# Kernel tuning notes

Hardware: AMD Instinct MI355X
Metric: run time of the kernel (lower is better)

The kernel has to match this reference:

```python
import jax, jax.numpy as jnp
import numpy as np

B, S, D, H = 4, 2048, 768, 12
HD = D // H
SCALE = HD ** -0.5


def setup_inputs() -> dict:
    key = jax.random.key(0)
    ks = jax.random.split(key, 9)
    std = D ** -0.5
    x = jax.random.normal(ks[0], (B, S, D), dtype=jnp.float32)
    Wq = jax.random.normal(ks[1], (D, D), dtype=jnp.float32) * std
    Wk = jax.random.normal(ks[2], (D, D), dtype=jnp.float32) * std
    Wv = jax.random.normal(ks[3], (D, D), dtype=jnp.float32) * std
    Wo = jax.random.normal(ks[4], (D, D), dtype=jnp.float32) * std
    bq = jax.random.normal(ks[5], (D,), dtype=jnp.float32) * 0.01
    bk = jax.random.normal(ks[6], (D,), dtype=jnp.float32) * 0.01
    bv = jax.random.normal(ks[7], (D,), dtype=jnp.float32) * 0.01
    bo = jax.random.normal(ks[8], (D,), dtype=jnp.float32) * 0.01
    return {"x": x, "Wq": Wq, "bq": bq, "Wk": Wk, "bk": bk,
            "Wv": Wv, "bv": bv, "Wo": Wo, "bo": bo}


def reference(x, Wq, bq, Wk, bk, Wv, bv, Wo, bo):
    b, s, _ = x.shape
    # projections (torch Linear: y = x @ W.T + b)
    q = (x @ Wq.T + bq).reshape(b, s, H, HD).transpose(0, 2, 1, 3)  # [B,H,S,HD]
    k = (x @ Wk.T + bk).reshape(b, s, H, HD).transpose(0, 2, 1, 3)
    v = (x @ Wv.T + bv).reshape(b, s, H, HD).transpose(0, 2, 1, 3)
    attn = jnp.einsum('bhqd,bhkd->bhqk', q, k) * SCALE
    attn = jax.nn.softmax(attn, axis=-1)  # dropout is identity in eval mode
    out = jnp.einsum('bhqk,bhkd->bhqd', attn, v)
    out = out.transpose(0, 2, 1, 3).reshape(b, s, D)
    return out @ Wo.T + bo
```

## Files before the change

### kernel.cpp

```cpp
#include <hip/hip_runtime.h>

#define LOG2E 1.4426950408889634f
#define QSCALE (0.125f * LOG2E)

typedef __attribute__((ext_vector_type(8))) __bf16 bf8_t;
typedef __attribute__((ext_vector_type(4))) float f4_t;

__device__ __forceinline__ unsigned short f2bf(float f) {
  unsigned int u = __float_as_uint(f);
  u += 0x7fff + ((u >> 16) & 1);
  return (unsigned short)(u >> 16);
}

__device__ __forceinline__ void async16(const void* g, void* l) {
  __builtin_amdgcn_global_load_lds(
      (const __attribute__((address_space(1))) void*)g,
      (__attribute__((address_space(3))) void*)l, 16, 0, 0);
}

__device__ __forceinline__ int swm(int r) {
  return ((r & 3) << 4) | ((r & 8) << 3);
}
__device__ __forceinline__ int swzoff(int row, int cb) {
  return (row << 7) + (cb ^ swm(row));
}

__global__ void cvt_multi(const float* __restrict__ x,
                          const float* __restrict__ w0, const float* __restrict__ w1,
                          const float* __restrict__ w2, const float* __restrict__ w3,
                          unsigned short* __restrict__ xb,
                          unsigned short* __restrict__ d0, unsigned short* __restrict__ d1,
                          unsigned short* __restrict__ d2, unsigned short* __restrict__ d3) {
  const int NX = 1572864;
  const int NW = 147456;
  const int total = NX + 4 * NW;
  int i = blockIdx.x * blockDim.x + threadIdx.x;
  int stride = gridDim.x * blockDim.x;
  for (; i < total; i += stride) {
    const float* s;
    unsigned short* d;
    int off;
    if (i < NX) {
      s = x; d = xb; off = i;
    } else {
      int j = i - NX;
      int wsel = j / NW;
      off = j - wsel * NW;
      s = (wsel == 0) ? w0 : (wsel == 1) ? w1 : (wsel == 2) ? w2 : w3;
      d = (wsel == 0) ? d0 : (wsel == 1) ? d1 : (wsel == 2) ? d2 : d3;
    }
    float4 v = ((const float4*)s)[off];
    ushort4 o;
    o.x = f2bf(v.x); o.y = f2bf(v.y); o.z = f2bf(v.z); o.w = f2bf(v.w);
    ((ushort4*)d)[off] = o;
  }
}

__device__ __forceinline__ void gemm_core(const unsigned short* __restrict__ A,
                                          const unsigned short* __restrict__ Bm,
                                          int i0, int j0, char* ls,
                                          f4_t (&acc)[4][4]) {
  const int tid = threadIdx.x;
  const int l = tid & 63;
  const int wi = (tid >> 6) >> 1, wj = (tid >> 6) & 1;
  auto stage = [&](int buf, int k0) {
    char* dA = ls + buf * 32768;
    char* dB = dA + 16384;
#pragma unroll
    for (int u = 0; u < 4; ++u) {
      int p = (u * 256 + tid) * 16;
      int r = p >> 7, c = (p & 127) ^ swm(r);
      async16((const char*)A + ((size_t)(i0 + r) * 768 + k0) * 2 + c, dA + p);
      async16((const char*)Bm + ((size_t)(j0 + r) * 768 + k0) * 2 + c, dB + p);
    }
  };
  stage(0, 0);
  for (int kk = 0; kk < 12; ++kk) {
    if (kk < 11) {
      stage((kk + 1) & 1, (kk + 1) * 64);
      asm volatile("s_waitcnt vmcnt(8)" ::: "memory");
    } else {
      asm volatile("s_waitcnt vmcnt(0)" ::: "memory");
    }
    __builtin_amdgcn_s_barrier();
    const char* lsA = ls + (kk & 1) * 32768;
    const char* lsB = lsA + 16384;
#pragma unroll
    for (int ks = 0; ks < 2; ++ks) {
      bf8_t af[4], bfr[4];
#pragma unroll
      for (int mi = 0; mi < 4; ++mi)
        af[mi] = *(const bf8_t*)(lsA + swzoff(wi * 64 + mi * 16 + (l & 15),
                                              ks * 64 + ((l >> 4) << 4)));
#pragma unroll
      for (int nj = 0; nj < 4; ++nj)
        bfr[nj] = *(const bf8_t*)(lsB + swzoff(wj * 64 + nj * 16 + (l & 15),
                                               ks * 64 + ((l >> 4) << 4)));
      __builtin_amdgcn_s_setprio(1);
#pragma unroll
      for (int mi = 0; mi < 4; ++mi)
#pragma unroll
        for (int nj = 0; nj < 4; ++nj)
          acc[mi][nj] = __builtin_amdgcn_mfma_f32_16x16x32_bf16(
              af[mi], bfr[nj], acc[mi][nj], 0, 0, 0);
      __builtin_amdgcn_s_setprio(0);
    }
    __builtin_amdgcn_s_barrier();
  }
}

__global__ __launch_bounds__(256) void proj_qkv(
    const unsigned short* __restrict__ xb,
    const unsigned short* __restrict__ wq,
    const unsigned short* __restrict__ wk,
    const unsigned short* __restrict__ wv,
    const float* __restrict__ bq, const float* __restrict__ bk,
    const float* __restrict__ bv,
    unsigned short* __restrict__ qo, unsigned short* __restrict__ ko,
    unsigned short* __restrict__ vto) {
  __shared__ char ls[65536];
  const int bx = (blockIdx.x & 7) * 144 + (blockIdx.x >> 3);
  const int mt = bx / 18, nt = bx % 18;
  const int sec = nt / 6, nn = nt % 6;
  const int nbase = nn * 128;
  const int mbase = mt * 128;
  const unsigned short *A, *Bm;
  if (sec == 0)      { A = wq; Bm = xb; }
  else if (sec == 1) { A = wk; Bm = xb; }
  else               { A = xb; Bm = wv; }
  const int gi0 = (sec == 2) ? mbase : nbase;
  const int gj0 = (sec == 2) ? nbase : mbase;
  f4_t acc[4][4] = {};
  gemm_core(A, Bm, gi0, gj0, ls, acc);

  const int tid = threadIdx.x, l = tid & 63;
  const int wi = (tid >> 6) >> 1, wj = (tid >> 6) & 1;
#pragma unroll
  for (int mi = 0; mi < 4; ++mi) {
#pragma unroll
    for (int nj = 0; nj < 4; ++nj) {
      int ib = wi * 64 + mi * 16 + ((l >> 4) << 2);
      int j  = wj * 64 + nj * 16 + (l & 15);
      f4_t v = acc[mi][nj];
      ushort4 o;
      if (sec < 2) {
        const float* bias = sec ? bk : bq;
        float sc = sec ? 1.0f : QSCALE;
        float4 bs = *(const float4*)(bias + nbase + ib);
        o.x = f2bf((v[0] + bs.x) * sc);
        o.y = f2bf((v[1] + bs.y) * sc);
        o.z = f2bf((v[2] + bs.z) * sc);
        o.w = f2bf((v[3] + bs.w) * sc);
      } else {
        float bvs = bv[nbase + j];
        o.x = f2bf(v[0] + bvs); o.y = f2bf(v[1] + bvs);
        o.z = f2bf(v[2] + bvs); o.w = f2bf(v[3] + bvs);
      }
      int chunk = (ib >> 3) ^ (j & 15);
      *(ushort4*)(ls + j * 256 + chunk * 16 + ((ib & 7) << 1)) = o;
    }
  }
  __syncthreads();
  const int row = tid >> 1, half = tid & 1;
  if (sec < 2) {
    int sg = mbase + row;
    int b = sg >> 11, s = sg & 2047;
    int h = nn * 2 + half;
    unsigned short* dst = (sec ? ko : qo) + (((size_t)(b * 12 + h) * 2048 + s) << 6);
#pragma unroll
    for (int c = 0; c < 8; ++c) {
      int cb = half * 8 + c;
      uint4 v = *(const uint4*)(ls + row * 256 + ((cb ^ (row & 15)) << 4));
      ((uint4*)dst)[c] = v;
    }
  } else {
    int h = nn * 2 + (row >> 6), dh = row & 63;
    int b = mt >> 4;
    int scol = (mt & 15) * 128 + half * 64;
    unsigned short* dst = vto + ((size_t)((b * 12 + h) * 64 + dh)) * 2048 + scol;
#pragma unroll
    for (int c = 0; c < 8; ++c) {
      int cb = half * 8 + c;
      uint4 v = *(const uint4*)(ls + row * 256 + ((cb ^ (row & 15)) << 4));
      ((uint4*)dst)[c] = v;
    }
  }
}

__global__ __launch_bounds__(256) void proj_o(
    const unsigned short* __restrict__ attnb, const unsigned short* __restrict__ wo,
    const float* __restrict__ bo, float* __restrict__ outp) {
  __shared__ char ls[65536];
  const int bx = (blockIdx.x & 7) * 48 + (blockIdx.x >> 3);
  const int it = bx % 6, jt = bx / 6;
  const int i0 = it * 128, j0 = jt * 128;
  f4_t acc[4][4] = {};
  gemm_core(wo, attnb, i0, j0, ls, acc);
  const int tid = threadIdx.x, l = tid & 63;
  const int wi = (tid >> 6) >> 1, wj = (tid >> 6) & 1;
#pragma unroll
  for (int mi = 0; mi < 4; ++mi) {
#pragma unroll
    for (int nj = 0; nj < 4; ++nj) {
      int ib = i0 + wi * 64 + mi * 16 + ((l >> 4) << 2);
      int j  = j0 + wj * 64 + nj * 16 + (l & 15);
      float4 bs = *(const float4*)(bo + ib);
      float4 o;
      o.x = acc[mi][nj][0] + bs.x;
      o.y = acc[mi][nj][1] + bs.y;
      o.z = acc[mi][nj][2] + bs.z;
      o.w = acc[mi][nj][3] + bs.w;
      *(float4*)(outp + (size_t)j * 768 + ib) = o;
    }
  }
}

__global__ __launch_bounds__(512) void attn_kernel(
    const unsigned short* __restrict__ qg,
    const unsigned short* __restrict__ kg,
    const unsigned short* __restrict__ vtg,
    unsigned short* __restrict__ attnb) {
  __shared__ char ls[65536];
  const int tid = threadIdx.x, l = tid & 63, w = tid >> 6;
  const int qw = w & 3, hf = w >> 2;
  const int swz = (blockIdx.x & 7) * 96 + (blockIdx.x >> 3);
  const int q0 = (swz & 15) * 128;
  const int bh = swz >> 4;
  const size_t qkbase = (size_t)bh * 2048 * 64;
  const size_t vtbase = (size_t)bh * 64 * 2048;

#pragma unroll
  for (int u = 0; u < 2; ++u) {
    int p = (u * 512 + tid) * 16;
    int r = p >> 7, cb = p & 127;
    int c = cb ^ swm(r);
    async16((const char*)qg + (qkbase + (size_t)(q0 + r) * 64) * 2 + c, ls + p);
  }
  __syncthreads();
  bf8_t qf[2][2];
#pragma unroll
  for (int qt = 0; qt < 2; ++qt)
#pragma unroll
    for (int ks = 0; ks < 2; ++ks)
      qf[qt][ks] = *(const bf8_t*)(ls + swzoff(qw * 32 + qt * 16 + (l & 15),
                                               ks * 64 + ((l >> 4) << 4)));
  __syncthreads();

  const int p16 = tid * 16;
  const int sr = p16 >> 7;
  const int sc = (p16 & 127) ^ swm(sr);
  async16((const char*)kg + (qkbase + (size_t)sr * 64) * 2 + sc, ls + p16);
  async16((const char*)vtg + (vtbase + (size_t)sr * 2048) * 2 + sc,
          ls + 8192 + p16);
  async16((const char*)kg + (qkbase + (size_t)(64 + sr) * 64) * 2 + sc,
          ls + 16384 + p16);
  async16((const char*)vtg + (vtbase + (size_t)sr * 2048 + 64) * 2 + sc,
          ls + 16384 + 8192 + p16);
  const char* gKa = (const char*)kg + (qkbase + (size_t)(128 + sr) * 64) * 2 + sc;
  const char* gVa = (const char*)vtg + (vtbase + (size_t)sr * 2048 + 128) * 2 + sc;
  const char* gKb = gKa + 8192;
  const char* gVb = gVa + 128;

  int koff[4][2];
#pragma unroll
  for (int kt = 0; kt < 4; ++kt) {
    int i = l & 15;
    int row = ((kt >> 1) << 5) + ((kt & 1) << 2) + ((i >> 2) << 3) + (i & 3);
#pragma unroll
    for (int ks = 0; ks < 2; ++ks)
      koff[kt][ks] = swzoff(row, ks * 64 + ((l >> 4) << 4));
  }
  int voff[4][2];
#pragma unroll
  for (int dt = 0; dt < 4; ++dt)
#pragma unroll
    for (int ks = 0; ks < 2; ++ks)
      voff[dt][ks] = swzoff(dt * 16 + (l & 15), ks * 64 + ((l >> 4) << 4));

  bf8_t onesf;
#pragma unroll
  for (int e = 0; e < 8; ++e) onesf[e] = (__bf16)1.0f;

  f4_t acc[4][2] = {};
  f4_t accs[2] = {};

  for (int i = 0; i < 16; ++i) {
    if (i < 15) {
      char* dst = ls + (((i + 1) & 1) * 2) * 16384;
      async16(gKa, dst + p16);
      async16(gVa, dst + 8192 + p16);
      async16(gKb, dst + 16384 + p16);
      async16(gVb, dst + 16384 + 8192 + p16);
      gKa += 16384; gKb += 16384;
      gVa += 256;   gVb += 256;
      asm volatile("s_waitcnt vmcnt(4)" ::: "memory");
    } else {
      asm volatile("s_waitcnt vmcnt(0)" ::: "memory");
    }
    __builtin_amdgcn_s_barrier();
    const char* bK = ls + ((i & 1) * 2 + hf) * 16384;
    const char* bV = bK + 8192;

    f4_t sacc[4][2] = {};
    __builtin_amdgcn_s_setprio(1);
#pragma unroll
    for (int kt = 0; kt < 4; ++kt)
#pragma unroll
      for (int ks = 0; ks < 2; ++ks) {
        bf8_t a = *(const bf8_t*)(bK + koff[kt][ks]);
#pragma unroll
        for (int qt = 0; qt < 2; ++qt)
          sacc[kt][qt] = __builtin_amdgcn_mfma_f32_16x16x32_bf16(
              a, qf[qt][ks], sacc[kt][qt], 0, 0, 0);
      }
    __builtin_amdgcn_s_setprio(0);

    bf8_t pf[2][2];
#pragma unroll
    for (int qt = 0; qt < 2; ++qt)
#pragma unroll
      for (int ks = 0; ks < 2; ++ks)
#pragma unroll
        for (int e = 0; e < 8; ++e)
          pf[ks][qt][e] =
              (__bf16)__builtin_amdgcn_exp2f(sacc[2 * ks + (e >> 2)][qt][e & 3]);

    __builtin_amdgcn_s_setprio(1);
#pragma unroll
    for (int dt = 0; dt < 4; ++dt) {
      bf8_t av0 = *(const bf8_t*)(bV + voff[dt][0]);
      bf8_t av1 = *(const bf8_t*)(bV + voff[dt][1]);
#pragma unroll
      for (int qt = 0; qt < 2; ++qt) {
        acc[dt][qt] = __builtin_amdgcn_mfma_f32_16x16x32_bf16(av0, pf[0][qt],
                                                              acc[dt][qt], 0, 0, 0);
        acc[dt][qt] = __builtin_amdgcn_mfma_f32_16x16x32_bf16(av1, pf[1][qt],
                                                              acc[dt][qt], 0, 0, 0);
      }
    }
#pragma unroll
    for (int qt = 0; qt < 2; ++qt) {
      accs[qt] = __builtin_amdgcn_mfma_f32_16x16x32_bf16(onesf, pf[0][qt],
                                                         accs[qt], 0, 0, 0);
      accs[qt] = __builtin_amdgcn_mfma_f32_16x16x32_bf16(onesf, pf[1][qt],
                                                         accs[qt], 0, 0, 0);
    }
    __builtin_amdgcn_s_setprio(0);
    __builtin_amdgcn_s_barrier();
  }

  char* reg_ = ls + qw * 8704;
  if (hf) {
#pragma unroll
    for (int dt = 0; dt < 4; ++dt)
#pragma unroll
      for (int qt = 0; qt < 2; ++qt)
        *(f4_t*)(reg_ + (((dt * 2 + qt) * 64) + l) * 16) = acc[dt][qt];
    *(float2*)(reg_ + 8192 + l * 8) = float2{accs[0][0], accs[1][0]};
  }
  __syncthreads();
  if (!hf) {
    const int bb = bh / 12, h = bh % 12;
    float2 os = *(const float2*)(reg_ + 8192 + l * 8);
    float inv0 = 1.0f / (accs[0][0] + os.x);
    float inv1 = 1.0f / (accs[1][0] + os.y);
#pragma unroll
    for (int qt = 0; qt < 2; ++qt) {
      float inv = qt ? inv1 : inv0;
      int s = q0 + qw * 32 + qt * 16 + (l & 15);
#pragma unroll
      for (int dt = 0; dt < 4; ++dt) {
        f4_t other = *(const f4_t*)(reg_ + (((dt * 2 + qt) * 64) + l) * 16);
        int dg = h * 64 + dt * 16 + ((l >> 4) << 2);
        ushort4 o;
        o.x = f2bf((acc[dt][qt][0] + other[0]) * inv);
        o.y = f2bf((acc[dt][qt][1] + other[1]) * inv);
        o.z = f2bf((acc[dt][qt][2] + other[2]) * inv);
        o.w = f2bf((acc[dt][qt][3] + other[3]) * inv);
        *(ushort4*)(attnb + ((size_t)(bb * 2048 + s)) * 768 + dg) = o;
      }
    }
  }
}

extern "C" void kernel_launch(void* const* d_in, const int* in_sizes, int n_in,
                              void* d_out, int out_size, void* d_ws, size_t ws_size,
                              hipStream_t stream) {
  const float* x  = (const float*)d_in[0];
  const float* Wq = (const float*)d_in[1];
  const float* bq = (const float*)d_in[2];
  const float* Wk = (const float*)d_in[3];
  const float* bk = (const float*)d_in[4];
  const float* Wv = (const float*)d_in[5];
  const float* bv = (const float*)d_in[6];
  const float* Wo = (const float*)d_in[7];
  const float* bo = (const float*)d_in[8];

  const size_t XB_ELEMS = (size_t)8192 * 768;
  const size_t W_ELEMS  = (size_t)768 * 768;
  unsigned short* xb  = (unsigned short*)d_ws;
  unsigned short* wqb = xb  + XB_ELEMS;
  unsigned short* wkb = wqb + W_ELEMS;
  unsigned short* wvb = wkb + W_ELEMS;
  unsigned short* wob = wvb + W_ELEMS;
  unsigned short* qb  = wob + W_ELEMS;
  unsigned short* kb  = qb  + XB_ELEMS;
  unsigned short* vtb = kb  + XB_ELEMS;
  unsigned short* attnb = xb;

  cvt_multi<<<2048, 256, 0, stream>>>(x, Wq, Wk, Wv, Wo,
                                      xb, wqb, wkb, wvb, wob);
  proj_qkv<<<1152, 256, 0, stream>>>(xb, wqb, wkb, wvb, bq, bk, bv, qb, kb, vtb);
  attn_kernel<<<768, 512, 0, stream>>>(qb, kb, vtb, attnb);
  proj_o<<<384, 256, 0, stream>>>(attnb, wob, bo, (float*)d_out);
}
```

Before: 137.2 us.

## Software-pipeline softmax and PV across iterations for second-half waves

Waves with hf set now compute QK scores for the current tile and buffer them with V fragments in registers, then run exp2 and PV for the previous tile in the next iteration. The other half keeps the original order, so the two wave groups sit in different phases and their MFMA and transcendental work can interleave. In exchange the hf waves hold extra registers for the previous scores and V fragments, which can hurt occupancy, and the loop gains a drain step after it ends.

```diff
diff --git a/kernel.cpp b/kernel.cpp
--- a/kernel.cpp
+++ b/kernel.cpp
@@ -283,6 +283,39 @@
 
   f4_t acc[4][2] = {};
   f4_t accs[2] = {};
+  f4_t psacc[4][2];
+  bf8_t pvf[4][2];
+
+  auto do_sm = [&](f4_t (&sc)[4][2], bf8_t (&pf)[2][2]) {
+#pragma unroll
+    for (int qt = 0; qt < 2; ++qt)
+#pragma unroll
+      for (int ks = 0; ks < 2; ++ks)
+#pragma unroll
+        for (int e = 0; e < 8; ++e)
+          pf[ks][qt][e] =
+              (__bf16)__builtin_amdgcn_exp2f(sc[2 * ks + (e >> 2)][qt][e & 3]);
+  };
+  auto do_pv = [&](bf8_t (&pf)[2][2], bf8_t (&av)[4][2]) {
+    __builtin_amdgcn_s_setprio(1);
+#pragma unroll
+    for (int dt = 0; dt < 4; ++dt)
+#pragma unroll
+      for (int qt = 0; qt < 2; ++qt) {
+        acc[dt][qt] = __builtin_amdgcn_mfma_f32_16x16x32_bf16(av[dt][0], pf[0][qt],
+                                                              acc[dt][qt], 0, 0, 0);
+        acc[dt][qt] = __builtin_amdgcn_mfma_f32_16x16x32_bf16(av[dt][1], pf[1][qt],
+                                                              acc[dt][qt], 0, 0, 0);
+      }
+#pragma unroll
+    for (int qt = 0; qt < 2; ++qt) {
+      accs[qt] = __builtin_amdgcn_mfma_f32_16x16x32_bf16(onesf, pf[0][qt],
+                                                         accs[qt], 0, 0, 0);
+      accs[qt] = __builtin_amdgcn_mfma_f32_16x16x32_bf16(onesf, pf[1][qt],
+                                                         accs[qt], 0, 0, 0);
+    }
+    __builtin_amdgcn_s_setprio(0);
+  };
 
   for (int i = 0; i < 16; ++i) {
     if (i < 15) {
@@ -301,52 +334,64 @@
     const char* bK = ls + ((i & 1) * 2 + hf) * 16384;
     const char* bV = bK + 8192;
 
-    f4_t sacc[4][2] = {};
-    __builtin_amdgcn_s_setprio(1);
-#pragma unroll
-    for (int kt = 0; kt < 4; ++kt)
-#pragma unroll
-      for (int ks = 0; ks < 2; ++ks) {
-        bf8_t a = *(const bf8_t*)(bK + koff[kt][ks]);
+    if (!hf) {
+      f4_t sacc[4][2] = {};
+      __builtin_amdgcn_s_setprio(1);
+#pragma unroll
+      for (int kt = 0; kt < 4; ++kt)
+#pragma unroll
+        for (int ks = 0; ks < 2; ++ks) {
+          bf8_t a = *(const bf8_t*)(bK + koff[kt][ks]);
+#pragma unroll
+          for (int qt = 0; qt < 2; ++qt)
+            sacc[kt][qt] = __builtin_amdgcn_mfma_f32_16x16x32_bf16(
+                a, qf[qt][ks], sacc[kt][qt], 0, 0, 0);
+        }
+      __builtin_amdgcn_s_setprio(0);
+      bf8_t pf[2][2];
+      do_sm(sacc, pf);
+      bf8_t av[4][2];
+#pragma unroll
+      for (int dt = 0; dt < 4; ++dt) {
+        av[dt][0] = *(const bf8_t*)(bV + voff[dt][0]);
+        av[dt][1] = *(const bf8_t*)(bV + voff[dt][1]);
+      }
+      do_pv(pf, av);
+    } else {
+      if (i > 0) {
+        bf8_t pf[2][2];
+        do_sm(psacc, pf);
+        do_pv(pf, pvf);
+      }
+#pragma unroll
+      for (int kt = 0; kt < 4; ++kt)
 #pragma unroll
         for (int qt = 0; qt < 2; ++qt)
-          sacc[kt][qt] = __builtin_amdgcn_mfma_f32_16x16x32_bf16(
-              a, qf[qt][ks], sacc[kt][qt], 0, 0, 0);
-      }
-    __builtin_amdgcn_s_setprio(0);
-
+          psacc[kt][qt] = f4_t{0.0f, 0.0f, 0.0f, 0.0f};
+      __builtin_amdgcn_s_setprio(1);
+#pragma unroll
+      for (int kt = 0; kt < 4; ++kt)
+#pragma unroll
+        for (int ks = 0; ks < 2; ++ks) {
+          bf8_t a = *(const bf8_t*)(bK + koff[kt][ks]);
+#pragma unroll
+          for (int qt = 0; qt < 2; ++qt)
+            psacc[kt][qt] = __builtin_amdgcn_mfma_f32_16x16x32_bf16(
+                a, qf[qt][ks], psacc[kt][qt], 0, 0, 0);
+        }
+      __builtin_amdgcn_s_setprio(0);
+#pragma unroll
+      for (int dt = 0; dt < 4; ++dt) {
+        pvf[dt][0] = *(const bf8_t*)(bV + voff[dt][0]);
+        pvf[dt][1] = *(const bf8_t*)(bV + voff[dt][1]);
+      }
+    }
+    __builtin_amdgcn_s_barrier();
+  }
+  if (hf) {
     bf8_t pf[2][2];
-#pragma unroll
-    for (int qt = 0; qt < 2; ++qt)
-#pragma unroll
-      for (int ks = 0; ks < 2; ++ks)
-#pragma unroll
-        for (int e = 0; e < 8; ++e)
-          pf[ks][qt][e] =
-              (__bf16)__builtin_amdgcn_exp2f(sacc[2 * ks + (e >> 2)][qt][e & 3]);
-
-    __builtin_amdgcn_s_setprio(1);
-#pragma unroll
-    for (int dt = 0; dt < 4; ++dt) {
-      bf8_t av0 = *(const bf8_t*)(bV + voff[dt][0]);
-      bf8_t av1 = *(const bf8_t*)(bV + voff[dt][1]);
-#pragma unroll
-      for (int qt = 0; qt < 2; ++qt) {
-        acc[dt][qt] = __builtin_amdgcn_mfma_f32_16x16x32_bf16(av0, pf[0][qt],
-                                                              acc[dt][qt], 0, 0, 0);
-        acc[dt][qt] = __builtin_amdgcn_mfma_f32_16x16x32_bf16(av1, pf[1][qt],
-                                                              acc[dt][qt], 0, 0, 0);
-      }
-    }
-#pragma unroll
-    for (int qt = 0; qt < 2; ++qt) {
-      accs[qt] = __builtin_amdgcn_mfma_f32_16x16x32_bf16(onesf, pf[0][qt],
-                                                         accs[qt], 0, 0, 0);
-      accs[qt] = __builtin_amdgcn_mfma_f32_16x16x32_bf16(onesf, pf[1][qt],
-                                                         accs[qt], 0, 0, 0);
-    }
-    __builtin_amdgcn_s_setprio(0);
-    __builtin_amdgcn_s_barrier();
+    do_sm(psacc, pf);
+    do_pv(pf, pvf);
   }
 
   char* reg_ = ls + qw * 8704;
```

Measured after the change: 149.1 us. +8.7%, slower.

## Retile output projection to 128x64 with double-buffered pipeline; simplify attention sync

Applied to the files above, without the earlier changes.

The output projection now uses 128x64 tiles, doubling the grid to 768 blocks for better load balance across CUs. It replaces the shared gemm_core with an inline double-buffered async-to-LDS K-loop that uses less LDS. The attention loop drops its explicit vmcnt wait and top-of-loop barrier, relying on a __syncthreads after the prologue and at the end of each iteration. Smaller tiles give less operand reuse per block. The sync change depends on __syncthreads draining outstanding LDS-direct loads, which may also stall on the prefetch earlier than before.

```diff
diff --git a/kernel.cpp b/kernel.cpp
--- a/kernel.cpp
+++ b/kernel.cpp
@@ -190,20 +190,68 @@
 __global__ __launch_bounds__(256) void proj_o(
     const unsigned short* __restrict__ attnb, const unsigned short* __restrict__ wo,
     const float* __restrict__ bo, float* __restrict__ outp) {
-  __shared__ char ls[65536];
-  const int bx = (blockIdx.x & 7) * 48 + (blockIdx.x >> 3);
+  __shared__ char ls[49152];
+  const int bx = (blockIdx.x & 7) * 96 + (blockIdx.x >> 3);
   const int it = bx % 6, jt = bx / 6;
-  const int i0 = it * 128, j0 = jt * 128;
-  f4_t acc[4][4] = {};
-  gemm_core(wo, attnb, i0, j0, ls, acc);
+  const int i0 = it * 128, j0 = jt * 64;
   const int tid = threadIdx.x, l = tid & 63;
   const int wi = (tid >> 6) >> 1, wj = (tid >> 6) & 1;
+  auto stage = [&](int buf, int k0) {
+    char* dA = ls + buf * 24576;
+    char* dB = dA + 16384;
+#pragma unroll
+    for (int u = 0; u < 4; ++u) {
+      int p = (u * 256 + tid) * 16;
+      int r = p >> 7, c = (p & 127) ^ swm(r);
+      async16((const char*)wo + ((size_t)(i0 + r) * 768 + k0) * 2 + c, dA + p);
+    }
+#pragma unroll
+    for (int u = 0; u < 2; ++u) {
+      int p = (u * 256 + tid) * 16;
+      int r = p >> 7, c = (p & 127) ^ swm(r);
+      async16((const char*)attnb + ((size_t)(j0 + r) * 768 + k0) * 2 + c, dB + p);
+    }
+  };
+  f4_t acc[4][2] = {};
+  stage(0, 0);
+  for (int kk = 0; kk < 12; ++kk) {
+    if (kk < 11) {
+      stage((kk + 1) & 1, (kk + 1) * 64);
+      asm volatile("s_waitcnt vmcnt(6)" ::: "memory");
+    } else {
+      asm volatile("s_waitcnt vmcnt(0)" ::: "memory");
+    }
+    __builtin_amdgcn_s_barrier();
+    const char* lsA = ls + (kk & 1) * 24576;
+    const char* lsB = lsA + 16384;
+#pragma unroll
+    for (int ks = 0; ks < 2; ++ks) {
+      bf8_t af[4], bfr[2];
+#pragma unroll
+      for (int mi = 0; mi < 4; ++mi)
+        af[mi] = *(const bf8_t*)(lsA + swzoff(wi * 64 + mi * 16 + (l & 15),
+                                              ks * 64 + ((l >> 4) << 4)));
+#pragma unroll
+      for (int nj = 0; nj < 2; ++nj)
+        bfr[nj] = *(const bf8_t*)(lsB + swzoff(wj * 32 + nj * 16 + (l & 15),
+                                               ks * 64 + ((l >> 4) << 4)));
+      __builtin_amdgcn_s_setprio(1);
+#pragma unroll
+      for (int mi = 0; mi < 4; ++mi)
+#pragma unroll
+        for (int nj = 0; nj < 2; ++nj)
+          acc[mi][nj] = __builtin_amdgcn_mfma_f32_16x16x32_bf16(
+              af[mi], bfr[nj], acc[mi][nj], 0, 0, 0);
+      __builtin_amdgcn_s_setprio(0);
+    }
+    __builtin_amdgcn_s_barrier();
+  }
 #pragma unroll
   for (int mi = 0; mi < 4; ++mi) {
 #pragma unroll
-    for (int nj = 0; nj < 4; ++nj) {
+    for (int nj = 0; nj < 2; ++nj) {
       int ib = i0 + wi * 64 + mi * 16 + ((l >> 4) << 2);
-      int j  = j0 + wj * 64 + nj * 16 + (l & 15);
+      int j  = j0 + wj * 32 + nj * 16 + (l & 15);
       float4 bs = *(const float4*)(bo + ib);
       float4 o;
       o.x = acc[mi][nj][0] + bs.x;
@@ -260,6 +308,7 @@
   const char* gVa = (const char*)vtg + (vtbase + (size_t)sr * 2048 + 128) * 2 + sc;
   const char* gKb = gKa + 8192;
   const char* gVb = gVa + 128;
+  __syncthreads();
 
   int koff[4][2];
 #pragma unroll
@@ -293,11 +342,7 @@
       async16(gVb, dst + 16384 + 8192 + p16);
       gKa += 16384; gKb += 16384;
       gVa += 256;   gVb += 256;
-      asm volatile("s_waitcnt vmcnt(4)" ::: "memory");
-    } else {
-      asm volatile("s_waitcnt vmcnt(0)" ::: "memory");
-    }
-    __builtin_amdgcn_s_barrier();
+    }
     const char* bK = ls + ((i & 1) * 2 + hf) * 16384;
     const char* bV = bK + 8192;
 
@@ -346,7 +391,7 @@
                                                          accs[qt], 0, 0, 0);
     }
     __builtin_amdgcn_s_setprio(0);
-    __builtin_amdgcn_s_barrier();
+    __syncthreads();
   }
 
   char* reg_ = ls + qw * 8704;
@@ -412,5 +457,5 @@
                                       xb, wqb, wkb, wvb, wob);
   proj_qkv<<<1152, 256, 0, stream>>>(xb, wqb, wkb, wvb, bq, bk, bv, qb, kb, vtb);
   attn_kernel<<<768, 512, 0, stream>>>(qb, kb, vtb, attnb);
-  proj_o<<<384, 256, 0, stream>>>(attnb, wob, bo, (float*)d_out);
-}
+  proj_o<<<768, 256, 0, stream>>>(attnb, wob, bo, (float*)d_out);
+}
```

After: 133.8 us. 1.02x faster.

## Shrink projection GEMM tiles to 128x64 and simplify attention loop synchronisation

Applied to the files above, without the earlier changes.

The QKV and output projection GEMMs move from 128x128 to 128x64 output tiles. That doubles the grid sizes, cuts shared memory per block from 64KB to 48KB and remaps the Q/K/V^T epilogue stores for the narrower tile. The aim is better occupancy and load balance across CUs, at the cost of less operand reuse per block. Separately, the attention loop drops its explicit vmcnt wait and barrier before compute and relies on a full __syncthreads at the end of each iteration, plus one before the loop. This makes correctness depend on __syncthreads draining outstanding async LDS loads.

```diff
diff --git a/kernel.cpp b/kernel.cpp
--- a/kernel.cpp
+++ b/kernel.cpp
@@ -56,21 +56,25 @@
   }
 }
 
-__device__ __forceinline__ void gemm_core(const unsigned short* __restrict__ A,
-                                          const unsigned short* __restrict__ Bm,
-                                          int i0, int j0, char* ls,
-                                          f4_t (&acc)[4][4]) {
-  const int tid = threadIdx.x;
-  const int l = tid & 63;
+__device__ __forceinline__ void gemm_core64(const unsigned short* __restrict__ A,
+                                            const unsigned short* __restrict__ Bm,
+                                            int i0, int j0, char* ls,
+                                            f4_t (&acc)[4][2]) {
+  const int tid = threadIdx.x, l = tid & 63;
   const int wi = (tid >> 6) >> 1, wj = (tid >> 6) & 1;
   auto stage = [&](int buf, int k0) {
-    char* dA = ls + buf * 32768;
+    char* dA = ls + buf * 24576;
     char* dB = dA + 16384;
 #pragma unroll
     for (int u = 0; u < 4; ++u) {
       int p = (u * 256 + tid) * 16;
       int r = p >> 7, c = (p & 127) ^ swm(r);
       async16((const char*)A + ((size_t)(i0 + r) * 768 + k0) * 2 + c, dA + p);
+    }
+#pragma unroll
+    for (int u = 0; u < 2; ++u) {
+      int p = (u * 256 + tid) * 16;
+      int r = p >> 7, c = (p & 127) ^ swm(r);
       async16((const char*)Bm + ((size_t)(j0 + r) * 768 + k0) * 2 + c, dB + p);
     }
   };
@@ -78,29 +82,29 @@
   for (int kk = 0; kk < 12; ++kk) {
     if (kk < 11) {
       stage((kk + 1) & 1, (kk + 1) * 64);
-      asm volatile("s_waitcnt vmcnt(8)" ::: "memory");
+      asm volatile("s_waitcnt vmcnt(6)" ::: "memory");
     } else {
       asm volatile("s_waitcnt vmcnt(0)" ::: "memory");
     }
     __builtin_amdgcn_s_barrier();
-    const char* lsA = ls + (kk & 1) * 32768;
+    const char* lsA = ls + (kk & 1) * 24576;
     const char* lsB = lsA + 16384;
 #pragma unroll
     for (int ks = 0; ks < 2; ++ks) {
-      bf8_t af[4], bfr[4];
+      bf8_t af[4], bfr[2];
 #pragma unroll
       for (int mi = 0; mi < 4; ++mi)
         af[mi] = *(const bf8_t*)(lsA + swzoff(wi * 64 + mi * 16 + (l & 15),
                                               ks * 64 + ((l >> 4) << 4)));
 #pragma unroll
-      for (int nj = 0; nj < 4; ++nj)
-        bfr[nj] = *(const bf8_t*)(lsB + swzoff(wj * 64 + nj * 16 + (l & 15),
+      for (int nj = 0; nj < 2; ++nj)
+        bfr[nj] = *(const bf8_t*)(lsB + swzoff(wj * 32 + nj * 16 + (l & 15),
                                                ks * 64 + ((l >> 4) << 4)));
       __builtin_amdgcn_s_setprio(1);
 #pragma unroll
       for (int mi = 0; mi < 4; ++mi)
 #pragma unroll
-        for (int nj = 0; nj < 4; ++nj)
+        for (int nj = 0; nj < 2; ++nj)
           acc[mi][nj] = __builtin_amdgcn_mfma_f32_16x16x32_bf16(
               af[mi], bfr[nj], acc[mi][nj], 0, 0, 0);
       __builtin_amdgcn_s_setprio(0);
@@ -118,41 +122,42 @@
     const float* __restrict__ bv,
     unsigned short* __restrict__ qo, unsigned short* __restrict__ ko,
     unsigned short* __restrict__ vto) {
-  __shared__ char ls[65536];
-  const int bx = (blockIdx.x & 7) * 144 + (blockIdx.x >> 3);
+  __shared__ char ls[49152];
+  const int bx = (blockIdx.x & 7) * 288 + (blockIdx.x >> 3);
   const int mt = bx / 18, nt = bx % 18;
   const int sec = nt / 6, nn = nt % 6;
-  const int nbase = nn * 128;
-  const int mbase = mt * 128;
-  const unsigned short *A, *Bm;
-  if (sec == 0)      { A = wq; Bm = xb; }
-  else if (sec == 1) { A = wk; Bm = xb; }
-  else               { A = xb; Bm = wv; }
-  const int gi0 = (sec == 2) ? mbase : nbase;
-  const int gj0 = (sec == 2) ? nbase : mbase;
-  f4_t acc[4][4] = {};
-  gemm_core(A, Bm, gi0, gj0, ls, acc);
+  f4_t acc[4][2] = {};
+  int i0, j0;
+  if (sec < 2) {
+    i0 = nn * 128;
+    j0 = mt * 64;
+    gemm_core64(sec ? wk : wq, xb, i0, j0, ls, acc);
+  } else {
+    i0 = (mt >> 1) * 128;
+    j0 = (nn * 2 + (mt & 1)) * 64;
+    gemm_core64(xb, wv, i0, j0, ls, acc);
+  }
 
   const int tid = threadIdx.x, l = tid & 63;
   const int wi = (tid >> 6) >> 1, wj = (tid >> 6) & 1;
 #pragma unroll
   for (int mi = 0; mi < 4; ++mi) {
 #pragma unroll
-    for (int nj = 0; nj < 4; ++nj) {
+    for (int nj = 0; nj < 2; ++nj) {
       int ib = wi * 64 + mi * 16 + ((l >> 4) << 2);
-      int j  = wj * 64 + nj * 16 + (l & 15);
+      int j  = wj * 32 + nj * 16 + (l & 15);
       f4_t v = acc[mi][nj];
       ushort4 o;
       if (sec < 2) {
         const float* bias = sec ? bk : bq;
         float sc = sec ? 1.0f : QSCALE;
-        float4 bs = *(const float4*)(bias + nbase + ib);
+        float4 bs = *(const float4*)(bias + i0 + ib);
         o.x = f2bf((v[0] + bs.x) * sc);
         o.y = f2bf((v[1] + bs.y) * sc);
         o.z = f2bf((v[2] + bs.z) * sc);
         o.w = f2bf((v[3] + bs.w) * sc);
       } else {
-        float bvs = bv[nbase + j];
+        float bvs = bv[j0 + j];
         o.x = f2bf(v[0] + bvs); o.y = f2bf(v[1] + bvs);
         o.z = f2bf(v[2] + bvs); o.w = f2bf(v[3] + bvs);
       }
@@ -161,28 +166,29 @@
     }
   }
   __syncthreads();
-  const int row = tid >> 1, half = tid & 1;
+  const int row = tid >> 2, q4 = tid & 3;
   if (sec < 2) {
-    int sg = mbase + row;
+    int sg = mt * 64 + row;
     int b = sg >> 11, s = sg & 2047;
-    int h = nn * 2 + half;
-    unsigned short* dst = (sec ? ko : qo) + (((size_t)(b * 12 + h) * 2048 + s) << 6);
-#pragma unroll
-    for (int c = 0; c < 8; ++c) {
-      int cb = half * 8 + c;
+    unsigned short* base = sec ? ko : qo;
+#pragma unroll
+    for (int cc = 0; cc < 4; ++cc) {
+      int cb = q4 * 4 + cc;
       uint4 v = *(const uint4*)(ls + row * 256 + ((cb ^ (row & 15)) << 4));
-      ((uint4*)dst)[c] = v;
+      int h = nn * 2 + (cb >> 3);
+      *(uint4*)(base + (((size_t)(b * 12 + h) * 2048 + s) << 6) + (cb & 7) * 8) = v;
     }
   } else {
-    int h = nn * 2 + (row >> 6), dh = row & 63;
-    int b = mt >> 4;
-    int scol = (mt & 15) * 128 + half * 64;
-    unsigned short* dst = vto + ((size_t)((b * 12 + h) * 64 + dh)) * 2048 + scol;
-#pragma unroll
-    for (int c = 0; c < 8; ++c) {
-      int cb = half * 8 + c;
+    int h = nn * 2 + (mt & 1), dh = row;
+    int st = mt >> 1;
+    int b = st >> 4;
+    int sl = (st & 15) * 128;
+    unsigned short* dst0 = vto + ((size_t)((b * 12 + h) * 64 + dh)) * 2048 + sl;
+#pragma unroll
+    for (int cc = 0; cc < 4; ++cc) {
+      int cb = q4 * 4 + cc;
       uint4 v = *(const uint4*)(ls + row * 256 + ((cb ^ (row & 15)) << 4));
-      ((uint4*)dst)[c] = v;
+      *(uint4*)(dst0 + cb * 8) = v;
     }
   }
 }
@@ -190,20 +196,20 @@
 __global__ __launch_bounds__(256) void proj_o(
     const unsigned short* __restrict__ attnb, const unsigned short* __restrict__ wo,
     const float* __restrict__ bo, float* __restrict__ outp) {
-  __shared__ char ls[65536];
-  const int bx = (blockIdx.x & 7) * 48 + (blockIdx.x >> 3);
+  __shared__ char ls[49152];
+  const int bx = (blockIdx.x & 7) * 96 + (blockIdx.x >> 3);
   const int it = bx % 6, jt = bx / 6;
-  const int i0 = it * 128, j0 = jt * 128;
-  f4_t acc[4][4] = {};
-  gemm_core(wo, attnb, i0, j0, ls, acc);
+  const int i0 = it * 128, j0 = jt * 64;
+  f4_t acc[4][2] = {};
+  gemm_core64(wo, attnb, i0, j0, ls, acc);
   const int tid = threadIdx.x, l = tid & 63;
   const int wi = (tid >> 6) >> 1, wj = (tid >> 6) & 1;
 #pragma unroll
   for (int mi = 0; mi < 4; ++mi) {
 #pragma unroll
-    for (int nj = 0; nj < 4; ++nj) {
+    for (int nj = 0; nj < 2; ++nj) {
       int ib = i0 + wi * 64 + mi * 16 + ((l >> 4) << 2);
-      int j  = j0 + wj * 64 + nj * 16 + (l & 15);
+      int j  = j0 + wj * 32 + nj * 16 + (l & 15);
       float4 bs = *(const float4*)(bo + ib);
       float4 o;
       o.x = acc[mi][nj][0] + bs.x;
@@ -260,6 +266,7 @@
   const char* gVa = (const char*)vtg + (vtbase + (size_t)sr * 2048 + 128) * 2 + sc;
   const char* gKb = gKa + 8192;
   const char* gVb = gVa + 128;
+  __syncthreads();
 
   int koff[4][2];
 #pragma unroll
@@ -293,11 +300,7 @@
       async16(gVb, dst + 16384 + 8192 + p16);
       gKa += 16384; gKb += 16384;
       gVa += 256;   gVb += 256;
-      asm volatile("s_waitcnt vmcnt(4)" ::: "memory");
-    } else {
-      asm volatile("s_waitcnt vmcnt(0)" ::: "memory");
-    }
-    __builtin_amdgcn_s_barrier();
+    }
     const char* bK = ls + ((i & 1) * 2 + hf) * 16384;
     const char* bV = bK + 8192;
 
@@ -346,7 +349,7 @@
                                                          accs[qt], 0, 0, 0);
     }
     __builtin_amdgcn_s_setprio(0);
-    __builtin_amdgcn_s_barrier();
+    __syncthreads();
   }
 
   char* reg_ = ls + qw * 8704;
@@ -410,7 +413,7 @@
 
   cvt_multi<<<2048, 256, 0, stream>>>(x, Wq, Wk, Wv, Wo,
                                       xb, wqb, wkb, wvb, wob);
-  proj_qkv<<<1152, 256, 0, stream>>>(xb, wqb, wkb, wvb, bq, bk, bv, qb, kb, vtb);
+  proj_qkv<<<2304, 256, 0, stream>>>(xb, wqb, wkb, wvb, bq, bk, bv, qb, kb, vtb);
   attn_kernel<<<768, 512, 0, stream>>>(qb, kb, vtb, attnb);
-  proj_o<<<384, 256, 0, stream>>>(attnb, wob, bo, (float*)d_out);
-}
+  proj_o<<<768, 256, 0, stream>>>(attnb, wob, bo, (float*)d_out);
+}
```

Result: faster. 130.1 us (-5.1%).
